# Performance work log

Hardware: AMD Instinct MI355X
Metric: run time of the kernel (lower is better)

Reference implementation:

```python
import jax, jax.numpy as jnp
import numpy as np
import math

NUM_HEADS = 8
WINDOW = 8  # stage=1


def _windowed_attention(q, kv, Wq, bq, Wk, bk, Wv, bv, Wo, bo):
    B, N, C = q.shape
    H = W = int(math.isqrt(N))
    nh, ws = NUM_HEADS, WINDOW
    hd = C // nh
    scale = hd ** -0.5

    qp = q @ Wq + bq   # (B, N, C)
    kp = kv @ Wk + bk
    vp = kv @ Wv + bv

    def to_windows(x):
        # (B, N, C) -> (B, nh, nWh*nWw, ws*ws, hd)
        x = x.reshape(B, H // ws, ws, W // ws, ws, nh, hd)
        x = x.transpose(0, 5, 1, 3, 2, 4, 6)  # B, nh, nWh, nWw, ws, ws, hd
        return x.reshape(B, nh, (H // ws) * (W // ws), ws * ws, hd)

    qw = to_windows(qp)
    kw = to_windows(kp)
    vw = to_windows(vp)

    attn = jnp.einsum('bhnqd,bhnkd->bhnqk', qw, kw) * scale
    attn = jax.nn.softmax(attn.astype(jnp.float32), axis=-1).astype(qw.dtype)
    ow = jnp.einsum('bhnqk,bhnkd->bhnqd', attn, vw)

    # window reverse: (B, nh, nW, ws*ws, hd) -> (B, N, C)
    ow = ow.reshape(B, nh, H // ws, W // ws, ws, ws, hd)
    ow = ow.transpose(0, 2, 4, 3, 5, 1, 6)  # B, nWh, ws, nWw, ws, nh, hd
    x = ow.reshape(B, N, C)

    return x @ Wo + bo


def setup_inputs() -> dict:
    key = jax.random.key(0)
    ks = jax.random.split(key, 7)
    B, N, C = 4, 16384, 256
    s = 1.0 / math.sqrt(C)
    return {
        'q': jax.random.normal(ks[0], (B, N, C), jnp.float32),
        'kv': jax.random.normal(ks[1], (B, N, C), jnp.float32),
        'Wq': jax.random.normal(ks[2], (C, C), jnp.float32) * s,
        'bq': jnp.zeros((C,), jnp.float32),
        'Wk': jax.random.normal(ks[3], (C, C), jnp.float32) * s,
        'bk': jnp.zeros((C,), jnp.float32),
        'Wv': jax.random.normal(ks[4], (C, C), jnp.float32) * s,
        'bv': jnp.zeros((C,), jnp.float32),
        'Wo': jax.random.normal(ks[5], (C, C), jnp.float32) * s,
        'bo': jnp.zeros((C,), jnp.float32),
    }


def reference(q, kv, Wq, bq, Wk, bk, Wv, bv, Wo, bo):
    return _windowed_attention(q, kv, Wq, bq, Wk, bk, Wv, bv, Wo, bo)
```

## Files before the change

### kernel.cpp

```cpp
#include <hip/hip_runtime.h>
#include <hip/hip_bf16.h>

typedef __bf16 bf16;
typedef __bf16 bf16x8 __attribute__((ext_vector_type(8)));
typedef float  f32x4  __attribute__((ext_vector_type(4)));

#define DEVINL __device__ __forceinline__

DEVINL void gll16(const void* g, void* l) {
  __builtin_amdgcn_global_load_lds(
      (const __attribute__((address_space(1))) unsigned int*)g,
      (__attribute__((address_space(3))) unsigned int*)l, 16, 0, 0);
}

__global__ void k_prep(const float* __restrict__ Wq, const float* __restrict__ Wk,
                       const float* __restrict__ Wv, const float* __restrict__ Wo,
                       bf16* __restrict__ packQ, bf16* __restrict__ packO) {
  const int n = threadIdx.x;
  const int k = blockIdx.x;
  const int m = blockIdx.y;
  const int kk = k & 63, iter4 = k >> 6;
  const int h = kk >> 5, kg = (kk >> 3) & 3, e = k & 7;
  if (m < 3) {
    const float* W = (m == 0) ? Wq : (m == 1) ? Wk : Wv;
    const bf16 v = (bf16)W[k * 256 + n];
    const int nglob = m * 256 + n;
    const int tile = nglob >> 7, row = nglob & 127;
    const int kgs = kg ^ ((row >> 1) & 3);
    packQ[(size_t)((tile * 4 + iter4) * 1024 + h * 512 + row * 4 + kgs) * 8 + e] = v;
  } else {
    const float w = Wo[k * 256 + n];
    const bf16 hi = (bf16)w;
    const bf16 v = (m == 3) ? hi : (bf16)(w - (float)hi);
    const int iter = (m - 3) * 4 + iter4;
    const int tile = n >> 7, row = n & 127;
    packO[(size_t)((tile * 8 + iter) * 1024 + h * 512 + row * 4 + kg) * 8 + e] = v;
  }
}

__global__ __launch_bounds__(256, 3) void k_qkv(
    const float* __restrict__ q, const float* __restrict__ kv,
    const bf16* __restrict__ packQ,
    const float* __restrict__ bq, const float* __restrict__ bk,
    const float* __restrict__ bvv,
    bf16* __restrict__ qp, bf16* __restrict__ kp, bf16* __restrict__ vp) {
  __shared__ __align__(16) bf16 Bs[2][2][128 * 32];

  const int g = blockIdx.x, xcd = g & 7, s = g >> 3;
  const int nb = s % 6, mh = s / 6;
  const int m0 = (mh * 8 + xcd) * 128;
  const float* A = (nb < 2) ? q : kv;

  const int tid = threadIdx.x, lane = tid & 63, wave = tid >> 6;
  const int lm = lane & 15, lq = lane >> 4;
  const int swzlq = lq ^ ((lm >> 1) & 3);
  const int mw = wave * 32;

  f32x4 acc[2][8];
#pragma unroll
  for (int t = 0; t < 2; ++t)
#pragma unroll
    for (int nf = 0; nf < 8; ++nf) acc[t][nf] = (f32x4)0.0f;

  const bf16* pbase = packQ + (size_t)nb * 4 * 8192;
  const float* arow0 = A + (size_t)(m0 + mw + lm) * 256 + lq * 8;
  const float* arow1 = arow0 + (size_t)16 * 256;

  float4 ar[2][2][2];

  auto stageB = [&](int it, int buf) {
    const bf16* pit = pbase + it * 8192;
#pragma unroll
    for (int u = 0; u < 4; ++u) {
      const int c = u * 256 + tid;
      bf16* dst = (u < 2) ? &Bs[buf][0][c * 8] : &Bs[buf][1][(c - 512) * 8];
      gll16(pit + c * 8, dst);
    }
  };
  auto loadA = [&](int it) {
#pragma unroll
    for (int t = 0; t < 2; ++t)
#pragma unroll
      for (int ks = 0; ks < 2; ++ks) {
        const float* p = (t == 0 ? arow0 : arow1) + it * 64 + ks * 32;
        ar[t][ks][0] = *(const float4*)(p);
        ar[t][ks][1] = *(const float4*)(p + 4);
      }
  };

  stageB(0, 0);
  loadA(0);
  __syncthreads();

#pragma unroll
  for (int i = 0; i < 4; ++i) {
    const int cur = i & 1;
    if (i < 3) stageB(i + 1, cur ^ 1);

    bf16x8 av[2][2];
#pragma unroll
    for (int t = 0; t < 2; ++t)
#pragma unroll
      for (int ks = 0; ks < 2; ++ks) {
        const float4 f0 = ar[t][ks][0], f1 = ar[t][ks][1];
        bf16x8 v;
        v[0] = (bf16)f0.x; v[1] = (bf16)f0.y; v[2] = (bf16)f0.z; v[3] = (bf16)f0.w;
        v[4] = (bf16)f1.x; v[5] = (bf16)f1.y; v[6] = (bf16)f1.z; v[7] = (bf16)f1.w;
        av[t][ks] = v;
      }
    if (i < 3) loadA(i + 1);

#pragma unroll
    for (int ks = 0; ks < 2; ++ks) {
      bf16x8 bvf[8];
#pragma unroll
      for (int nf = 0; nf < 8; ++nf)
        bvf[nf] = *(const bf16x8*)&Bs[cur][ks][(nf * 16 + lm) * 32 + swzlq * 8];
#pragma unroll
      for (int t = 0; t < 2; ++t)
#pragma unroll
        for (int nf = 0; nf < 8; ++nf)
          acc[t][nf] = __builtin_amdgcn_mfma_f32_16x16x32_bf16(av[t][ks], bvf[nf], acc[t][nf], 0, 0, 0);
    }
    if (i < 3) __syncthreads();
  }

  const int ncbase = (nb * 128) & 255;
  bf16* op = (nb < 2) ? qp : (nb < 4) ? kp : vp;
  const float* bp = (nb < 2) ? bq : (nb < 4) ? bk : bvv;
#pragma unroll
  for (int t = 0; t < 2; ++t)
#pragma unroll
    for (int nf = 0; nf < 8; ++nf) {
      const int nc = ncbase + nf * 16 + lm;
      const float bval = bp[nc];
#pragma unroll
      for (int r = 0; r < 4; ++r) {
        const int mg = m0 + mw + t * 16 + lq * 4 + r;
        op[(size_t)mg * 256 + nc] = (bf16)(acc[t][nf][r] + bval);
      }
    }
}

__global__ __launch_bounds__(256, 3) void k_oproj(
    const bf16* __restrict__ ao, const bf16* __restrict__ packO,
    const float* __restrict__ bo, float* __restrict__ out) {
  __shared__ __align__(16) bf16 As[2][128 * 32];
  __shared__ __align__(16) bf16 Bs[2][128 * 32];

  const int g = blockIdx.x, xcd = g & 7, s = g >> 3;
  const int nb = s & 1, mh = s >> 1;
  const int m0 = (mh * 8 + xcd) * 128;

  const int tid = threadIdx.x, lane = tid & 63, wave = tid >> 6;
  const int mw = (wave >> 1) * 64, nw = (wave & 1) * 64;
  const int lm = lane & 15, lq = lane >> 4;

  f32x4 acc[4][4];
#pragma unroll
  for (int a = 0; a < 4; ++a)
#pragma unroll
    for (int b = 0; b < 4; ++b) acc[a][b] = (f32x4)0.0f;

  const bf16* pbase = packO + (size_t)nb * 8 * 8192;

  for (int i = 0; i < 8; ++i) {
    const int kA = (i & 3) * 64;
#pragma unroll
    for (int u = 0; u < 4; ++u) {
      const int c = u * 256 + tid;
      const int h = c >> 9, r2 = c & 511;
      const int row = r2 >> 2, kg = c & 3;
      bf16* dstB = (u < 2) ? &Bs[0][c * 8] : &Bs[1][(c - 512) * 8];
      gll16(pbase + (size_t)i * 8192 + c * 8, dstB);
      bf16* dstA = (u < 2) ? &As[0][r2 * 8] : &As[1][r2 * 8];
      gll16(ao + (size_t)(m0 + row) * 256 + kA + h * 32 + kg * 8, dstA);
    }
    __syncthreads();
#pragma unroll
    for (int ks = 0; ks < 2; ++ks) {
      bf16x8 av[4], bvf[4];
#pragma unroll
      for (int t = 0; t < 4; ++t)
        av[t] = *(const bf16x8*)&As[ks][(mw + t * 16 + lm) * 32 + lq * 8];
#pragma unroll
      for (int t = 0; t < 4; ++t)
        bvf[t] = *(const bf16x8*)&Bs[ks][(nw + t * 16 + lm) * 32 + lq * 8];
#pragma unroll
      for (int a = 0; a < 4; ++a)
#pragma unroll
        for (int b = 0; b < 4; ++b)
          acc[a][b] = __builtin_amdgcn_mfma_f32_16x16x32_bf16(av[a], bvf[b], acc[a][b], 0, 0, 0);
    }
    __syncthreads();
  }

#pragma unroll
  for (int a = 0; a < 4; ++a)
#pragma unroll
    for (int b = 0; b < 4; ++b) {
      const int nglob = nb * 128 + nw + b * 16 + lm;
      const float bval = bo[nglob];
#pragma unroll
      for (int r = 0; r < 4; ++r) {
        const int mg = m0 + mw + a * 16 + lq * 4 + r;
        out[(size_t)mg * 256 + nglob] = acc[a][b][r] + bval;
      }
    }
}

__global__ __launch_bounds__(256) void k_attn(
    const bf16* __restrict__ qp, const bf16* __restrict__ kp,
    const bf16* __restrict__ vp, bf16* __restrict__ ao) {
  __shared__ __align__(16) bf16 smem[3 * 64 * 136];
  bf16* Qs = smem;
  bf16* Ks = smem + 64 * 136;
  bf16* Vs = smem + 2 * 64 * 136;
  bf16* Ps = smem;
  bf16* Os = Vs;

  const int tid = threadIdx.x;
  const int lane = tid & 63;
  const int hl = tid >> 6;
  const int bw = blockIdx.x;
  const int b = bw >> 8;
  const int w = bw & 255;
  const int wy = w >> 4, wx = w & 15;
  const int ch0 = blockIdx.y * 128;

#pragma unroll
  for (int i = 0; i < 4; ++i) {
    const int c = i * 256 + tid;
    const int t = c >> 4;
    const int off = (c & 15) * 8;
    const int ty = t >> 3, tx = t & 7;
    const size_t gr = ((size_t)(b * 128 + wy * 8 + ty)) * 128 + wx * 8 + tx;
    const size_t gi = gr * 256 + ch0 + off;
    const int li = t * 136 + off;
    *(uint4*)&Qs[li] = *(const uint4*)&qp[gi];
    *(uint4*)&Ks[li] = *(const uint4*)&kp[gi];
    *(uint4*)&Vs[li] = *(const uint4*)&vp[gi];
  }
  __syncthreads();

  const int chh = hl * 32;
  const int lm = lane & 15;
  const int lq = lane >> 4;

  bf16x8 qa[4], kb[4];
#pragma unroll
  for (int t = 0; t < 4; ++t)
    qa[t] = *(const bf16x8*)&Qs[(t * 16 + lm) * 136 + chh + lq * 8];
#pragma unroll
  for (int t = 0; t < 4; ++t)
    kb[t] = *(const bf16x8*)&Ks[(t * 16 + lm) * 136 + chh + lq * 8];

  f32x4 s[4][4];
#pragma unroll
  for (int i = 0; i < 4; ++i)
#pragma unroll
    for (int j = 0; j < 4; ++j) s[i][j] = (f32x4)0.0f;
#pragma unroll
  for (int i = 0; i < 4; ++i)
#pragma unroll
    for (int j = 0; j < 4; ++j)
      s[i][j] = __builtin_amdgcn_mfma_f32_16x16x32_bf16(qa[i], kb[j], s[i][j], 0, 0, 0);

  const float scale = 0.17677669529663687f;
  float rl[4][4];
#pragma unroll
  for (int mt = 0; mt < 4; ++mt) {
#pragma unroll
    for (int r = 0; r < 4; ++r) {
      float mx = fmaxf(fmaxf(s[mt][0][r], s[mt][1][r]), fmaxf(s[mt][2][r], s[mt][3][r]));
      mx = fmaxf(mx, __shfl_xor(mx, 1));
      mx = fmaxf(mx, __shfl_xor(mx, 2));
      mx = fmaxf(mx, __shfl_xor(mx, 4));
      mx = fmaxf(mx, __shfl_xor(mx, 8));
      float sum = 0.f;
#pragma unroll
      for (int nt = 0; nt < 4; ++nt) {
        const float p = __expf((s[mt][nt][r] - mx) * scale);
        s[mt][nt][r] = p;
        sum += p;
      }
      sum += __shfl_xor(sum, 1);
      sum += __shfl_xor(sum, 2);
      sum += __shfl_xor(sum, 4);
      sum += __shfl_xor(sum, 8);
      rl[mt][r] = 1.0f / sum;
    }
  }

  __syncthreads();

  bf16* Ph = Ps + hl * 4096;
#pragma unroll
  for (int mt = 0; mt < 4; ++mt)
#pragma unroll
    for (int nt = 0; nt < 4; ++nt)
#pragma unroll
      for (int r = 0; r < 4; ++r) {
        const int qrow = mt * 16 + lq * 4 + r;
        const int kcol = nt * 16 + lm;
        Ph[qrow * 64 + (((kcol >> 3) ^ (qrow & 7)) << 3) + (kcol & 7)] = (bf16)s[mt][nt][r];
      }

  f32x4 o[4][2];
#pragma unroll
  for (int i = 0; i < 4; ++i) { o[i][0] = (f32x4)0.0f; o[i][1] = (f32x4)0.0f; }
#pragma unroll
  for (int ks = 0; ks < 2; ++ks) {
    bf16x8 pa[4];
#pragma unroll
    for (int mt = 0; mt < 4; ++mt) {
      const int qrow = mt * 16 + lm;
      const int gsel = ks * 4 + lq;
      pa[mt] = *(const bf16x8*)&Ph[qrow * 64 + ((gsel ^ (qrow & 7)) << 3)];
    }
    bf16x8 vbf[2];
#pragma unroll
    for (int ntd = 0; ntd < 2; ++ntd) {
      const int d = ntd * 16 + lm;
      bf16x8 tv;
#pragma unroll
      for (int j = 0; j < 8; ++j)
        tv[j] = Vs[(ks * 32 + lq * 8 + j) * 136 + chh + d];
      vbf[ntd] = tv;
    }
#pragma unroll
    for (int mt = 0; mt < 4; ++mt)
#pragma unroll
      for (int ntd = 0; ntd < 2; ++ntd)
        o[mt][ntd] = __builtin_amdgcn_mfma_f32_16x16x32_bf16(pa[mt], vbf[ntd], o[mt][ntd], 0, 0, 0);
  }

  __syncthreads();

#pragma unroll
  for (int mt = 0; mt < 4; ++mt)
#pragma unroll
    for (int ntd = 0; ntd < 2; ++ntd)
#pragma unroll
      for (int r = 0; r < 4; ++r) {
        const int qrow = mt * 16 + lq * 4 + r;
        const int d = ntd * 16 + lm;
        Os[qrow * 136 + chh + d] = (bf16)(o[mt][ntd][r] * rl[mt][r]);
      }
  __syncthreads();

#pragma unroll
  for (int i = 0; i < 4; ++i) {
    const int c = i * 256 + tid;
    const int t = c >> 4;
    const int off = (c & 15) * 8;
    const int ty = t >> 3, tx = t & 7;
    const size_t gr = ((size_t)(b * 128 + wy * 8 + ty)) * 128 + wx * 8 + tx;
    *(uint4*)&ao[gr * 256 + ch0 + off] = *(const uint4*)&Os[t * 136 + off];
  }
}

extern "C" void kernel_launch(void* const* d_in, const int* in_sizes, int n_in,
                              void* d_out, int out_size, void* d_ws, size_t ws_size,
                              hipStream_t stream) {
  const float* q  = (const float*)d_in[0];
  const float* kv = (const float*)d_in[1];
  const float* Wq = (const float*)d_in[2];
  const float* bq = (const float*)d_in[3];
  const float* Wk = (const float*)d_in[4];
  const float* bk = (const float*)d_in[5];
  const float* Wv = (const float*)d_in[6];
  const float* bv = (const float*)d_in[7];
  const float* Wo = (const float*)d_in[8];
  const float* bo = (const float*)d_in[9];
  float* out = (float*)d_out;

  char* ws = (char*)d_ws;
  bf16* packQ = (bf16*)(ws + 0);
  bf16* packO = (bf16*)(ws + 393216);
  const size_t PLANE = (size_t)65536 * 256 * 2;
  bf16* qp = (bf16*)(ws + 1048576);
  bf16* kp = (bf16*)(ws + 1048576 + PLANE);
  bf16* vp = (bf16*)(ws + 1048576 + 2 * PLANE);
  bf16* ao = (bf16*)(ws + 1048576 + 3 * PLANE);
  if (ws_size < 1048576 + 4 * PLANE) return;

  k_prep<<<dim3(256, 5), 256, 0, stream>>>(Wq, Wk, Wv, Wo, packQ, packO);
  k_qkv<<<3072, 256, 0, stream>>>(q, kv, packQ, bq, bk, bv, qp, kp, vp);
  k_attn<<<dim3(1024, 2), 256, 0, stream>>>(qp, kp, vp, ao);
  k_oproj<<<1024, 256, 0, stream>>>(ao, packO, bo, out);
}
```

Measured before the change: 296.2 us.

## Double-buffer O-projection GEMM with register A operands and swizzled B tiles

Restructures the output-projection kernel so the A operand (attention output) is loaded straight from global memory into registers instead of staged through LDS. The B weight tiles are double-buffered in LDS so the next iteration's loads overlap the current MFMAs. The packed Wo layout gets an XOR swizzle to avoid LDS bank conflicts. The wave tiling changes to 32 rows by 128 columns per wave, and occupancy hints are raised for both GEMM kernels, which may increase register pressure or cause spills.

```diff
diff --git a/kernel.cpp b/kernel.cpp
--- a/kernel.cpp
+++ b/kernel.cpp
@@ -34,11 +34,12 @@
     const bf16 v = (m == 3) ? hi : (bf16)(w - (float)hi);
     const int iter = (m - 3) * 4 + iter4;
     const int tile = n >> 7, row = n & 127;
-    packO[(size_t)((tile * 8 + iter) * 1024 + h * 512 + row * 4 + kg) * 8 + e] = v;
-  }
-}
-
-__global__ __launch_bounds__(256, 3) void k_qkv(
+    const int kgs = kg ^ ((row >> 1) & 3);
+    packO[(size_t)((tile * 8 + iter) * 1024 + h * 512 + row * 4 + kgs) * 8 + e] = v;
+  }
+}
+
+__global__ __launch_bounds__(256, 5) void k_qkv(
     const float* __restrict__ q, const float* __restrict__ kv,
     const bf16* __restrict__ packQ,
     const float* __restrict__ bq, const float* __restrict__ bk,
@@ -142,69 +143,91 @@
     }
 }
 
-__global__ __launch_bounds__(256, 3) void k_oproj(
+__global__ __launch_bounds__(256, 4) void k_oproj(
     const bf16* __restrict__ ao, const bf16* __restrict__ packO,
     const float* __restrict__ bo, float* __restrict__ out) {
-  __shared__ __align__(16) bf16 As[2][128 * 32];
-  __shared__ __align__(16) bf16 Bs[2][128 * 32];
+  __shared__ __align__(16) bf16 Bs[2][2][128 * 32];
 
   const int g = blockIdx.x, xcd = g & 7, s = g >> 3;
   const int nb = s & 1, mh = s >> 1;
   const int m0 = (mh * 8 + xcd) * 128;
 
   const int tid = threadIdx.x, lane = tid & 63, wave = tid >> 6;
-  const int mw = (wave >> 1) * 64, nw = (wave & 1) * 64;
   const int lm = lane & 15, lq = lane >> 4;
-
-  f32x4 acc[4][4];
-#pragma unroll
-  for (int a = 0; a < 4; ++a)
-#pragma unroll
-    for (int b = 0; b < 4; ++b) acc[a][b] = (f32x4)0.0f;
+  const int swzlq = lq ^ ((lm >> 1) & 3);
+  const int mw = wave * 32;
+
+  f32x4 acc[2][8];
+#pragma unroll
+  for (int t = 0; t < 2; ++t)
+#pragma unroll
+    for (int nf = 0; nf < 8; ++nf) acc[t][nf] = (f32x4)0.0f;
 
   const bf16* pbase = packO + (size_t)nb * 8 * 8192;
-
-  for (int i = 0; i < 8; ++i) {
-    const int kA = (i & 3) * 64;
+  const bf16* arow0 = ao + (size_t)(m0 + mw + lm) * 256 + lq * 8;
+  const bf16* arow1 = arow0 + (size_t)16 * 256;
+
+  auto stageB = [&](int it, int buf) {
+    const bf16* pit = pbase + (size_t)it * 8192;
 #pragma unroll
     for (int u = 0; u < 4; ++u) {
       const int c = u * 256 + tid;
-      const int h = c >> 9, r2 = c & 511;
-      const int row = r2 >> 2, kg = c & 3;
-      bf16* dstB = (u < 2) ? &Bs[0][c * 8] : &Bs[1][(c - 512) * 8];
-      gll16(pbase + (size_t)i * 8192 + c * 8, dstB);
-      bf16* dstA = (u < 2) ? &As[0][r2 * 8] : &As[1][r2 * 8];
-      gll16(ao + (size_t)(m0 + row) * 256 + kA + h * 32 + kg * 8, dstA);
-    }
-    __syncthreads();
+      bf16* dst = (u < 2) ? &Bs[buf][0][c * 8] : &Bs[buf][1][(c - 512) * 8];
+      gll16(pit + c * 8, dst);
+    }
+  };
+
+  bf16x8 arA[2][2], arB[2][2];
+  auto loadA = [&](int it, bf16x8 (&dst)[2][2]) {
+    const int kA = (it & 3) * 64;
+#pragma unroll
+    for (int t = 0; t < 2; ++t)
+#pragma unroll
+      for (int ks = 0; ks < 2; ++ks)
+        dst[t][ks] = *(const bf16x8*)((t == 0 ? arow0 : arow1) + kA + ks * 32);
+  };
+  auto computeIter = [&](const bf16x8 (&av)[2][2], int cur) {
 #pragma unroll
     for (int ks = 0; ks < 2; ++ks) {
-      bf16x8 av[4], bvf[4];
-#pragma unroll
-      for (int t = 0; t < 4; ++t)
-        av[t] = *(const bf16x8*)&As[ks][(mw + t * 16 + lm) * 32 + lq * 8];
-#pragma unroll
-      for (int t = 0; t < 4; ++t)
-        bvf[t] = *(const bf16x8*)&Bs[ks][(nw + t * 16 + lm) * 32 + lq * 8];
-#pragma unroll
-      for (int a = 0; a < 4; ++a)
-#pragma unroll
-        for (int b = 0; b < 4; ++b)
-          acc[a][b] = __builtin_amdgcn_mfma_f32_16x16x32_bf16(av[a], bvf[b], acc[a][b], 0, 0, 0);
-    }
-    __syncthreads();
-  }
-
-#pragma unroll
-  for (int a = 0; a < 4; ++a)
-#pragma unroll
-    for (int b = 0; b < 4; ++b) {
-      const int nglob = nb * 128 + nw + b * 16 + lm;
+      bf16x8 bvf[8];
+#pragma unroll
+      for (int nf = 0; nf < 8; ++nf)
+        bvf[nf] = *(const bf16x8*)&Bs[cur][ks][(nf * 16 + lm) * 32 + swzlq * 8];
+#pragma unroll
+      for (int t = 0; t < 2; ++t)
+#pragma unroll
+        for (int nf = 0; nf < 8; ++nf)
+          acc[t][nf] = __builtin_amdgcn_mfma_f32_16x16x32_bf16(av[t][ks], bvf[nf], acc[t][nf], 0, 0, 0);
+    }
+  };
+
+  stageB(0, 0);
+  loadA(0, arA);
+  __syncthreads();
+
+#pragma unroll
+  for (int i = 0; i < 8; ++i) {
+    const int cur = i & 1;
+    if (i < 7) {
+      stageB(i + 1, cur ^ 1);
+      if (cur == 0) loadA(i + 1, arB);
+      else          loadA(i + 1, arA);
+    }
+    if (cur == 0) computeIter(arA, cur);
+    else          computeIter(arB, cur);
+    if (i < 7) __syncthreads();
+  }
+
+#pragma unroll
+  for (int t = 0; t < 2; ++t)
+#pragma unroll
+    for (int nf = 0; nf < 8; ++nf) {
+      const int nglob = nb * 128 + nf * 16 + lm;
       const float bval = bo[nglob];
 #pragma unroll
       for (int r = 0; r < 4; ++r) {
-        const int mg = m0 + mw + a * 16 + lq * 4 + r;
-        out[(size_t)mg * 256 + nglob] = acc[a][b][r] + bval;
+        const int mg = m0 + mw + t * 16 + lq * 4 + r;
+        out[(size_t)mg * 256 + nglob] = acc[t][nf][r] + bval;
       }
     }
 }
```

After: 602.1 us. 103% more time.
